# Kernel optimization log

Measured on AMD Instinct MI355X. Metric: run time of the kernel, lower is better.

The kernel has to match this reference:

```python
import jax, jax.numpy as jnp
import numpy as np

B, Wd, C, H, F = 48, 88, 256, 32, 1024
NH_SELF, NH_CROSS = 8, 8


def _ln(x, g, b, eps=1e-5):
    mu = x.mean(-1, keepdims=True)
    var = ((x - mu) ** 2).mean(-1, keepdims=True)
    return (x - mu) / jnp.sqrt(var + eps) * g + b


def setup_inputs() -> dict:
    key = jax.random.key(0)
    ks = jax.random.split(key, 16)
    s = 0.02  # weight init scale
    d = {
        'pooled_features': jax.random.normal(ks[0], (B, Wd, C), jnp.float32),
        'features': jax.random.normal(ks[1], (B, C, H, Wd), jnp.float32),
        'self_pe': jax.random.normal(ks[2], (Wd, C), jnp.float32),
        'cross_pe': jax.random.normal(ks[3], (H, C), jnp.float32),
    }
    # LayerNorm params
    for n in ['ln_qs', 'ln_vs', 'ln_qc', 'ln_kv', 'ln_vc', 'ln_ffn']:
        d[n + '_g'] = jnp.ones((C,), jnp.float32)
        d[n + '_b'] = jnp.zeros((C,), jnp.float32)
    # attention projections (stored [in,out]; y = x @ W + b)
    names = ['Wq_s', 'Wk_s', 'Wv_s', 'Wp_s', 'Wq_c', 'Wk_c', 'Wv_c', 'Wp_c']
    for i, n in enumerate(names):
        d[n] = jax.random.normal(ks[4 + i], (C, C), jnp.float32) * s
    for n in ['bq_s', 'bv_s', 'bp_s', 'bq_c', 'bv_c', 'bp_c']:
        d[n] = jnp.zeros((C,), jnp.float32)
    # FFN
    d['W1'] = jax.random.normal(ks[12], (C, F), jnp.float32) * s
    d['b1'] = jnp.zeros((F,), jnp.float32)
    d['W2'] = jax.random.normal(ks[13], (F, C), jnp.float32) * s
    d['b2'] = jnp.zeros((C,), jnp.float32)
    return d


def reference(pooled_features, features, self_pe, cross_pe,
              ln_qs_g, ln_qs_b, ln_vs_g, ln_vs_b,
              ln_qc_g, ln_qc_b, ln_kv_g, ln_kv_b, ln_vc_g, ln_vc_b,
              ln_ffn_g, ln_ffn_b,
              Wq_s, bq_s, Wk_s, Wv_s, bv_s, Wp_s, bp_s,
              Wq_c, bq_c, Wk_c, Wv_c, bv_c, Wp_c, bp_c,
              W1, b1, W2, b2):
    b, w, c = pooled_features.shape
    h = features.shape[2]
    ds = c // NH_SELF
    dc = c // NH_CROSS

    # ---- cross attention first (op_order='cross_first', with_pe=True) ----
    xq = pooled_features                                  # [B,W,C]
    qn = _ln(xq, ln_qc_g, ln_qc_b)
    kv = jnp.transpose(features, (0, 3, 2, 1))            # [B,W,H,C]
    kn = _ln(kv + cross_pe[None, None], ln_kv_g, ln_kv_b)
    vn = _ln(kv, ln_vc_g, ln_vc_b)
    q = (qn @ Wq_c + bq_c).reshape(b, w, NH_CROSS, dc)    # query len 1 per column
    k = (kn @ Wk_c).reshape(b, w, h, NH_CROSS, dc)
    v = (vn @ Wv_c + bv_c).reshape(b, w, h, NH_CROSS, dc)
    attn = jnp.einsum('bwhd,bwkhd->bwhk', q, k) * (dc ** -0.5)
    attn = jax.nn.softmax(attn, axis=-1)
    out = jnp.einsum('bwhk,bwkhd->bwhd', attn, v).reshape(b, w, c)
    x = out @ Wp_c + bp_c + xq

    # ---- self attention over width tokens ----
    qn = _ln(x + self_pe[None], ln_qs_g, ln_qs_b)
    vn = _ln(x, ln_vs_g, ln_vs_b)
    q = (qn @ Wq_s + bq_s).reshape(b, w, NH_SELF, ds)
    k = (qn @ Wk_s).reshape(b, w, NH_SELF, ds)
    v = (vn @ Wv_s + bv_s).reshape(b, w, NH_SELF, ds)
    attn = jnp.einsum('bnhd,bmhd->bhnm', q, k) * (ds ** -0.5)
    attn = jax.nn.softmax(attn, axis=-1)
    out = jnp.einsum('bhnm,bmhd->bnhd', attn, v).reshape(b, w, c)
    x = out @ Wp_s + bp_s + x

    # ---- FFN (mmcv FFN, num_fcs=2, GELU, identity residual) ----
    hdn = _ln(x, ln_ffn_g, ln_ffn_b)
    hdn = jax.nn.gelu(hdn @ W1 + b1, approximate=False) @ W2 + b2
    return x + hdn
```

## Files before the change

### kernel.cpp

```cpp
#include <hip/hip_runtime.h>
#include <math.h>

#define B_   48
#define W_   88
#define C_   256
#define H_   32
#define F_   1024
#define BW_  (B_ * W_)
#define BWH_ (B_ * W_ * H_)
#define HW_  (H_ * W_)

typedef float  f32x4  __attribute__((ext_vector_type(4)));
typedef __bf16 bf16x8 __attribute__((ext_vector_type(8)));

__device__ __forceinline__ unsigned short f2bf(float f) {
  union { float f; unsigned int u; } v; v.f = f;
  unsigned int r = v.u + 0x7FFFu + ((v.u >> 16) & 1u);
  return (unsigned short)(r >> 16);
}
__device__ __forceinline__ float bf2f(unsigned short h) {
  union { unsigned int u; float f; } v; v.u = ((unsigned int)h) << 16;
  return v.f;
}
__device__ __forceinline__ unsigned int pack2(float a, float b) {
  return (unsigned int)f2bf(a) | ((unsigned int)f2bf(b) << 16);
}

__global__ __launch_bounds__(256) void prep_all(
    const float* __restrict__ Wq_s, const float* __restrict__ Wk_s,
    const float* __restrict__ Wv_s, const float* __restrict__ Wp_s,
    const float* __restrict__ W1, const float* __restrict__ W2,
    const float* __restrict__ Wq_c, const float* __restrict__ Wk_c,
    const float* __restrict__ Wv_c, const float* __restrict__ Wp_c,
    const float* __restrict__ bq_s, const float* __restrict__ bv_s,
    const float* __restrict__ bq_c, const float* __restrict__ bv_c,
    const float* __restrict__ bp_c,
    const float* __restrict__ pooled,
    const float* __restrict__ ln_qc_g, const float* __restrict__ ln_qc_b,
    const float* __restrict__ cross_pe,
    unsigned short* __restrict__ wqkvs, unsigned short* __restrict__ wps,
    unsigned short* __restrict__ w1t, unsigned short* __restrict__ w2t,
    unsigned short* __restrict__ mqk, unsigned short* __restrict__ mvp,
    float* __restrict__ bqk, float* __restrict__ bvp,
    float* __restrict__ bqkvs, unsigned short* __restrict__ qn_c,
    float* __restrict__ pes) {
  __shared__ float smem[256 * 33 + 4 * 33];
  int blk = blockIdx.x, t = threadIdx.x;

  if (blk < 768) {
    const float* src; unsigned short* dst; int Cc, R, tile;
    if (blk < 64)       { src = Wq_s; dst = wqkvs;          Cc = 256;  R = 256;  tile = blk; }
    else if (blk < 128) { src = Wk_s; dst = wqkvs + 65536;  Cc = 256;  R = 256;  tile = blk - 64; }
    else if (blk < 192) { src = Wv_s; dst = wqkvs + 131072; Cc = 256;  R = 256;  tile = blk - 128; }
    else if (blk < 256) { src = Wp_s; dst = wps;            Cc = 256;  R = 256;  tile = blk - 192; }
    else if (blk < 512) { src = W1;   dst = w1t;            Cc = 1024; R = 256;  tile = blk - 256; }
    else                { src = W2;   dst = w2t;            Cc = 256;  R = 1024; tile = blk - 512; }
    int tcn = Cc >> 5;
    int tr = tile / tcn, tc = tile % tcn;
    float (*lds)[33] = (float(*)[33])smem;
    int r = t >> 3, c4 = (t & 7) * 4;
    float4 v = *(const float4*)(src + (size_t)(tr * 32 + r) * Cc + tc * 32 + c4);
    lds[r][c4 + 0] = v.x; lds[r][c4 + 1] = v.y; lds[r][c4 + 2] = v.z; lds[r][c4 + 3] = v.w;
    __syncthreads();
    int rd = t >> 3, cd4 = (t & 7) * 4;
    unsigned int u0 = pack2(lds[cd4 + 0][rd], lds[cd4 + 1][rd]);
    unsigned int u1 = pack2(lds[cd4 + 2][rd], lds[cd4 + 3][rd]);
    uint2 u; u.x = u0; u.y = u1;
    *(uint2*)(dst + (size_t)(tc * 32 + rd) * R + tr * 32 + cd4) = u;
  } else if (blk < 1280) {
    int lb = blk - 768;
    int h = lb >> 6, cb = lb & 63;
    float (*wq)[33] = (float(*)[33])smem;
    float (*wk)[33] = (float(*)[33])(smem + 256 * 33);
#pragma unroll
    for (int p = 0; p < 8; p++) {
      int dp = (t >> 3) + 32 * p, d4 = (t & 7) * 4;
      float4 v = *(const float4*)(Wq_c + (size_t)dp * 256 + 32 * h + d4);
      wq[dp][d4 + 0] = v.x; wq[dp][d4 + 1] = v.y; wq[dp][d4 + 2] = v.z; wq[dp][d4 + 3] = v.w;
    }
    if (t < 128) {
      int c_l = t >> 5, dd = t & 31;
      wk[c_l][dd] = Wk_c[(size_t)(cb * 4 + c_l) * 256 + 32 * h + dd];
    }
    __syncthreads();
    const float scale = 0.17677669529663689f;
    int c_l = t >> 6, ln = t & 63;
    int n = 256 * h + cb * 4 + c_l;
#pragma unroll
    for (int j = 0; j < 4; j++) {
      int dp = ln + 64 * j;
      float acc = 0.f;
#pragma unroll
      for (int dd = 0; dd < 32; dd++) acc += wq[dp][dd] * wk[c_l][dd];
      mqk[(size_t)n * 256 + dp] = f2bf(acc * scale);
    }
    if (ln == 0) {
      float bb = 0.f;
#pragma unroll
      for (int dd = 0; dd < 32; dd++) bb += bq_c[32 * h + dd] * wk[c_l][dd];
      bqk[n] = bb * scale;
    }
  } else if (blk < 1792) {
    int lb = blk - 1280;
    int h = lb >> 6, db = lb & 63;
    float (*wv)[33] = (float(*)[33])smem;
    float (*wp)[33] = (float(*)[33])(smem + 256 * 33);
#pragma unroll
    for (int p = 0; p < 8; p++) {
      int c = (t >> 3) + 32 * p, d4 = (t & 7) * 4;
      float4 v = *(const float4*)(Wv_c + (size_t)c * 256 + 32 * h + d4);
      wv[c][d4 + 0] = v.x; wv[c][d4 + 1] = v.y; wv[c][d4 + 2] = v.z; wv[c][d4 + 3] = v.w;
    }
    if (t < 128) {
      int d_l = t >> 5, dd = t & 31;
      wp[d_l][dd] = Wp_c[(size_t)(32 * h + dd) * 256 + db * 4 + d_l];
    }
    __syncthreads();
    int d_l = t >> 6, ln = t & 63;
    int d = db * 4 + d_l;
#pragma unroll
    for (int j = 0; j < 4; j++) {
      int c = ln + 64 * j;
      float acc = 0.f;
#pragma unroll
      for (int dd = 0; dd < 32; dd++) acc += wv[c][dd] * wp[d_l][dd];
      mvp[(size_t)d * 2048 + 256 * h + c] = f2bf(acc);
    }
  } else if (blk == 1792) {
    float acc = bp_c[t];
    for (int dp = 0; dp < 256; dp++) acc += bv_c[dp] * Wp_c[(size_t)dp * 256 + t];
    bvp[t] = acc;
    bqkvs[t] = bq_s[t]; bqkvs[256 + t] = 0.f; bqkvs[512 + t] = bv_s[t];
  } else if (blk < 6017) {
    int row = blk - 1793, c = t;
    float v = pooled[(size_t)row * C_ + c];
    float s1 = v, s2 = v * v;
#pragma unroll
    for (int m = 32; m > 0; m >>= 1) {
      s1 += __shfl_xor(s1, m, 64); s2 += __shfl_xor(s2, m, 64);
    }
    float* red = smem;
    int wave = c >> 6;
    if ((c & 63) == 0) { red[wave] = s1; red[4 + wave] = s2; }
    __syncthreads();
    s1 = red[0] + red[1] + red[2] + red[3];
    s2 = red[4] + red[5] + red[6] + red[7];
    float mu = s1 * (1.f / C_);
    float rs = rsqrtf(s2 * (1.f / C_) - mu * mu + 1e-5f);
    qn_c[(size_t)row * C_ + c] = f2bf((v - mu) * rs * ln_qc_g[c] + ln_qc_b[c]);
  } else {
    int h = t >> 3, seg = t & 7;
    const float* pr = cross_pe + (size_t)h * 256 + seg * 32;
    float s1 = 0.f, s2 = 0.f;
#pragma unroll
    for (int i = 0; i < 32; i++) { float v = pr[i]; s1 += v; s2 += v * v; }
    s1 += __shfl_xor(s1, 1, 8); s2 += __shfl_xor(s2, 1, 8);
    s1 += __shfl_xor(s1, 2, 8); s2 += __shfl_xor(s2, 2, 8);
    s1 += __shfl_xor(s1, 4, 8); s2 += __shfl_xor(s2, 4, 8);
    if (seg == 0) { pes[2 * h] = s1; pes[2 * h + 1] = s2; }
  }
}

__global__ __launch_bounds__(128, 2) void cross_fused(
    const float* __restrict__ features, const float* __restrict__ cross_pe,
    const unsigned short* __restrict__ qt_g,
    const float* __restrict__ g_kv, const float* __restrict__ b_kv,
    const float* __restrict__ g_vc, const float* __restrict__ b_vc,
    const float* __restrict__ pes,
    unsigned short* __restrict__ ctx_g) {
  __shared__ __attribute__((aligned(16))) float stage[2 * 4 * 268];
  const int p = blockIdx.x;
  const int xcd = p & 7, slot = p >> 3;
  const int b = xcd + 8 * (slot / 22);
  const int w0 = (slot % 22) * 4;
  const int t = threadIdx.x;
  const int bw0 = b * 88 + w0;
  const int w = t >> 5, c8 = t & 31, cbase = c8 << 3;

  float qg[8][8], Qg[8], Qb[8];
  {
    float gk8[8], bk8[8];
    float4 u0 = *(const float4*)(g_kv + cbase), u1 = *(const float4*)(g_kv + cbase + 4);
    gk8[0]=u0.x; gk8[1]=u0.y; gk8[2]=u0.z; gk8[3]=u0.w;
    gk8[4]=u1.x; gk8[5]=u1.y; gk8[6]=u1.z; gk8[7]=u1.w;
    u0 = *(const float4*)(b_kv + cbase); u1 = *(const float4*)(b_kv + cbase + 4);
    bk8[0]=u0.x; bk8[1]=u0.y; bk8[2]=u0.z; bk8[3]=u0.w;
    bk8[4]=u1.x; bk8[5]=u1.y; bk8[6]=u1.z; bk8[7]=u1.w;
    const unsigned short* qrow = qt_g + (size_t)(bw0 + w) * 2048 + cbase;
#pragma unroll
    for (int hd = 0; hd < 8; hd++) {
      bf16x8 qv = *(const bf16x8*)(qrow + hd * 256);
      float sg = 0.f, sb = 0.f;
#pragma unroll
      for (int i = 0; i < 8; i++) {
        float qf = (float)qv[i];
        qg[hd][i] = qf * gk8[i];
        sg += qg[hd][i];
        sb += qf * bk8[i];
      }
      Qg[hd] = sg; Qb[hd] = sb;
    }
#pragma unroll
    for (int m = 1; m < 32; m <<= 1) {
#pragma unroll
      for (int hd = 0; hd < 8; hd++) {
        Qg[hd] += __shfl_xor(Qg[hd], m, 32);
        Qb[hd] += __shfl_xor(Qb[hd], m, 32);
      }
    }
  }

  float accA[8][8];
  float accB[8], l[8];
#pragma unroll
  for (int hd = 0; hd < 8; hd++) {
    accB[hd] = 0.f; l[hd] = 0.f;
#pragma unroll
    for (int i = 0; i < 8; i++) accA[hd][i] = 0.f;
  }

  const float* fbase = features + (size_t)b * (C_ * HW_) + w0;
  float4 x0 = *(const float4*)(fbase + (size_t)t * HW_);
  float4 x1 = *(const float4*)(fbase + (size_t)(t + 128) * HW_);
  float4 y0 = *(const float4*)(fbase + (size_t)t * HW_ + 88);
  float4 y1 = *(const float4*)(fbase + (size_t)(t + 128) * HW_ + 88);

  float peC[8];
  {
    float4 q0 = *(const float4*)(cross_pe + cbase);
    float4 q1 = *(const float4*)(cross_pe + cbase + 4);
    peC[0]=q0.x; peC[1]=q0.y; peC[2]=q0.z; peC[3]=q0.w;
    peC[4]=q1.x; peC[5]=q1.y; peC[6]=q1.z; peC[7]=q1.w;
  }
  float pesC1 = pes[0], pesC2 = pes[1];

  float ps1, ps2, pu, pS[8], vprev[8];

  {
    float* st = stage;
    st[0 * 268 + t] = x0.x; st[1 * 268 + t] = x0.y;
    st[2 * 268 + t] = x0.z; st[3 * 268 + t] = x0.w;
    st[0 * 268 + 128 + t] = x1.x; st[1 * 268 + 128 + t] = x1.y;
    st[2 * 268 + 128 + t] = x1.z; st[3 * 268 + 128 + t] = x1.w;
    asm volatile("s_waitcnt lgkmcnt(0)" ::: "memory");
    __builtin_amdgcn_s_barrier();
    asm volatile("" ::: "memory");
    x0 = *(const float4*)(fbase + (size_t)t * HW_ + 2 * 88);
    x1 = *(const float4*)(fbase + (size_t)(t + 128) * HW_ + 2 * 88);
    const float* sr = st + w * 268 + cbase;
    float4 v0 = *(const float4*)(sr);
    float4 v1 = *(const float4*)(sr + 4);
    float vls[8] = {v0.x, v0.y, v0.z, v0.w, v1.x, v1.y, v1.z, v1.w};
    float peN[8];
    {
      float4 q0 = *(const float4*)(cross_pe + 256 + cbase);
      float4 q1 = *(const float4*)(cross_pe + 256 + cbase + 4);
      peN[0]=q0.x; peN[1]=q0.y; peN[2]=q0.z; peN[3]=q0.w;
      peN[4]=q1.x; peN[5]=q1.y; peN[6]=q1.z; peN[7]=q1.w;
    }
    float s1 = 0.f, s2 = 0.f, sp = 0.f, vp[8];
#pragma unroll
    for (int i = 0; i < 8; i++) {
      float v = vls[i];
      vp[i] = v + peC[i];
      s1 += v; s2 += v * v; sp += v * peC[i];
    }
#pragma unroll
    for (int hd = 0; hd < 8; hd++) {
      float a = 0.f;
#pragma unroll
      for (int i = 0; i < 8; i++) a += qg[hd][i] * vp[i];
      pS[hd] = a;
    }
    ps1 = s1; ps2 = s2; pu = s2 + 2.f * sp;
#pragma unroll
    for (int i = 0; i < 8; i++) vprev[i] = vls[i];
    float4 t0 = x0, t1 = x1;
    x0 = y0; x1 = y1; y0 = t0; y1 = t1;
#pragma unroll
    for (int i = 0; i < 8; i++) peC[i] = peN[i];
  }

  for (int h = 1; h < 32; ++h) {
    float* st = stage + (h & 1) * (4 * 268);
    st[0 * 268 + t] = x0.x; st[1 * 268 + t] = x0.y;
    st[2 * 268 + t] = x0.z; st[3 * 268 + t] = x0.w;
    st[0 * 268 + 128 + t] = x1.x; st[1 * 268 + 128 + t] = x1.y;
    st[2 * 268 + 128 + t] = x1.z; st[3 * 268 + 128 + t] = x1.w;
    asm volatile("s_waitcnt lgkmcnt(0)" ::: "memory");
    __builtin_amdgcn_s_barrier();
    asm volatile("" ::: "memory");
    if (h < 30) {
      x0 = *(const float4*)(fbase + (size_t)t * HW_ + (h + 2) * 88);
      x1 = *(const float4*)(fbase + (size_t)(t + 128) * HW_ + (h + 2) * 88);
    }
    const float* sr = st + w * 268 + cbase;
    float4 v0 = *(const float4*)(sr);
    float4 v1 = *(const float4*)(sr + 4);
#pragma unroll
    for (int m = 1; m < 32; m <<= 1) {
      ps1 += __shfl_xor(ps1, m, 32);
      ps2 += __shfl_xor(ps2, m, 32);
      pu  += __shfl_xor(pu, m, 32);
#pragma unroll
      for (int hd = 0; hd < 8; hd++) pS[hd] += __shfl_xor(pS[hd], m, 32);
    }
    float peN[8];
    if (h < 31) {
      float4 q0 = *(const float4*)(cross_pe + (h + 1) * 256 + cbase);
      float4 q1 = *(const float4*)(cross_pe + (h + 1) * 256 + cbase + 4);
      peN[0]=q0.x; peN[1]=q0.y; peN[2]=q0.z; peN[3]=q0.w;
      peN[4]=q1.x; peN[5]=q1.y; peN[6]=q1.z; peN[7]=q1.w;
    } else {
#pragma unroll
      for (int i = 0; i < 8; i++) peN[i] = 0.f;
    }
    float vls[8] = {v0.x, v0.y, v0.z, v0.w, v1.x, v1.y, v1.z, v1.w};
    float s1 = 0.f, s2 = 0.f, sp = 0.f, vp[8];
#pragma unroll
    for (int i = 0; i < 8; i++) {
      float v = vls[i];
      vp[i] = v + peC[i];
      s1 += v; s2 += v * v; sp += v * peC[i];
    }
    float nS[8];
#pragma unroll
    for (int hd = 0; hd < 8; hd++) {
      float a = 0.f;
#pragma unroll
      for (int i = 0; i < 8; i++) a += qg[hd][i] * vp[i];
      nS[hd] = a;
    }
    {
      float mu_v = ps1 * (1.f / 256.f);
      float rs_v = rsqrtf(ps2 * (1.f / 256.f) - mu_v * mu_v + 1e-5f);
      float mu_k = (ps1 + pesC1) * (1.f / 256.f);
      float rs_k = rsqrtf((pu + pesC2) * (1.f / 256.f) - mu_k * mu_k + 1e-5f);
#pragma unroll
      for (int hd = 0; hd < 8; hd++) {
        float sc = rs_k * (pS[hd] - mu_k * Qg[hd]) + Qb[hd];
        float e = __expf(sc);
        float er = e * rs_v;
        l[hd] += e;
        accB[hd] += er * mu_v;
#pragma unroll
        for (int i = 0; i < 8; i++) accA[hd][i] += er * vprev[i];
      }
    }
    ps1 = s1; ps2 = s2; pu = s2 + 2.f * sp;
#pragma unroll
    for (int hd = 0; hd < 8; hd++) pS[hd] = nS[hd];
#pragma unroll
    for (int i = 0; i < 8; i++) { vprev[i] = vls[i]; peC[i] = peN[i]; }
    pesC1 = pes[2 * h]; pesC2 = pes[2 * h + 1];
    float4 t0 = x0, t1 = x1;
    x0 = y0; x1 = y1; y0 = t0; y1 = t1;
  }

  {
#pragma unroll
    for (int m = 1; m < 32; m <<= 1) {
      ps1 += __shfl_xor(ps1, m, 32);
      ps2 += __shfl_xor(ps2, m, 32);
      pu  += __shfl_xor(pu, m, 32);
#pragma unroll
      for (int hd = 0; hd < 8; hd++) pS[hd] += __shfl_xor(pS[hd], m, 32);
    }
    float mu_v = ps1 * (1.f / 256.f);
    float rs_v = rsqrtf(ps2 * (1.f / 256.f) - mu_v * mu_v + 1e-5f);
    float mu_k = (ps1 + pesC1) * (1.f / 256.f);
    float rs_k = rsqrtf((pu + pesC2) * (1.f / 256.f) - mu_k * mu_k + 1e-5f);
#pragma unroll
    for (int hd = 0; hd < 8; hd++) {
      float sc = rs_k * (pS[hd] - mu_k * Qg[hd]) + Qb[hd];
      float e = __expf(sc);
      float er = e * rs_v;
      l[hd] += e;
      accB[hd] += er * mu_v;
#pragma unroll
      for (int i = 0; i < 8; i++) accA[hd][i] += er * vprev[i];
    }
  }

  float gv8[8], bv8[8];
  {
    float4 u0 = *(const float4*)(g_vc + cbase), u1 = *(const float4*)(g_vc + cbase + 4);
    gv8[0]=u0.x; gv8[1]=u0.y; gv8[2]=u0.z; gv8[3]=u0.w;
    gv8[4]=u1.x; gv8[5]=u1.y; gv8[6]=u1.z; gv8[7]=u1.w;
    u0 = *(const float4*)(b_vc + cbase); u1 = *(const float4*)(b_vc + cbase + 4);
    bv8[0]=u0.x; bv8[1]=u0.y; bv8[2]=u0.z; bv8[3]=u0.w;
    bv8[4]=u1.x; bv8[5]=u1.y; bv8[6]=u1.z; bv8[7]=u1.w;
  }
  unsigned short* orow = ctx_g + (size_t)(bw0 + w) * 2048 + cbase;
#pragma unroll
  for (int hd = 0; hd < 8; hd++) {
    float inv = 1.f / l[hd];
    unsigned short pk[8];
#pragma unroll
    for (int i = 0; i < 8; i++)
      pk[i] = f2bf(gv8[i] * (accA[hd][i] - accB[hd]) * inv + bv8[i]);
    *(uint4*)(orow + hd * 256) = *(uint4*)pk;
  }
}

__global__ __launch_bounds__(256) void ln_rows(
    const float* __restrict__ x,
    const float* __restrict__ g, const float* __restrict__ bta,
    unsigned short* __restrict__ out) {
  int row = blockIdx.x, c = threadIdx.x;
  float v = x[(size_t)row * C_ + c];
  float s1 = v, s2 = v * v;
#pragma unroll
  for (int m = 32; m > 0; m >>= 1) {
    s1 += __shfl_xor(s1, m, 64);
    s2 += __shfl_xor(s2, m, 64);
  }
  __shared__ float red[8];
  int wave = c >> 6;
  if ((c & 63) == 0) { red[wave] = s1; red[4 + wave] = s2; }
  __syncthreads();
  s1 = red[0] + red[1] + red[2] + red[3];
  s2 = red[4] + red[5] + red[6] + red[7];
  float mu = s1 * (1.f / C_);
  float rs = rsqrtf(s2 * (1.f / C_) - mu * mu + 1e-5f);
  out[(size_t)row * C_ + c] = f2bf((v - mu) * rs * g[c] + bta[c]);
}

__global__ __launch_bounds__(256) void ln_dual(
    const float* __restrict__ x, const float* __restrict__ pe,
    const float* __restrict__ g1, const float* __restrict__ b1a,
    const float* __restrict__ g2, const float* __restrict__ b2a,
    unsigned short* __restrict__ out1, unsigned short* __restrict__ out2) {
  int row = blockIdx.x, c = threadIdx.x;
  float v = x[(size_t)row * C_ + c];
  float vp = v + pe[(size_t)(row % 88) * C_ + c];
  float s1 = v, s2 = v * v, t1 = vp, t2 = vp * vp;
#pragma unroll
  for (int m = 32; m > 0; m >>= 1) {
    s1 += __shfl_xor(s1, m, 64); s2 += __shfl_xor(s2, m, 64);
    t1 += __shfl_xor(t1, m, 64); t2 += __shfl_xor(t2, m, 64);
  }
  __shared__ float red[16];
  int wave = c >> 6;
  if ((c & 63) == 0) {
    red[wave] = s1; red[4 + wave] = s2; red[8 + wave] = t1; red[12 + wave] = t2;
  }
  __syncthreads();
  s1 = red[0] + red[1] + red[2] + red[3];
  s2 = red[4] + red[5] + red[6] + red[7];
  t1 = red[8] + red[9] + red[10] + red[11];
  t2 = red[12] + red[13] + red[14] + red[15];
  float mu = s1 * (1.f / C_), rs = rsqrtf(s2 * (1.f / C_) - mu * mu + 1e-5f);
  float mup = t1 * (1.f / C_), rsp = rsqrtf(t2 * (1.f / C_) - mup * mup + 1e-5f);
  out1[(size_t)row * C_ + c] = f2bf((vp - mup) * rsp * g1[c] + b1a[c]);
  out2[(size_t)row * C_ + c] = f2bf((v - mu) * rs * g2[c] + b2a[c]);
}

__global__ __launch_bounds__(256) void gemm_bt(
    const unsigned short* __restrict__ A, const unsigned short* __restrict__ Bt,
    int M, int N, int K,
    const float* __restrict__ bias, const float* __restrict__ resid,
    float* __restrict__ outF, unsigned short* __restrict__ outB, int act_gelu) {
  __shared__ __attribute__((aligned(16))) unsigned short As[64][32];
  __shared__ __attribute__((aligned(16))) unsigned short Bs[64][32];
  const int tiles_n = N >> 6;
  const int bm = blockIdx.x / tiles_n;
  const int bn = blockIdx.x % tiles_n;
  const int tid = threadIdx.x;
  const int wave = tid >> 6, lane = tid & 63;
  const int quad = lane >> 4, lr = lane & 15;
  const int wm = (wave >> 1) << 5, wn = (wave & 1) << 5;
  const int lrow = tid >> 2;
  const int lcol = (tid & 3) << 3;
  const size_t a_base = (size_t)(bm * 64 + lrow) * K + lcol;
  const size_t b_base = (size_t)(bn * 64 + lrow) * K + lcol;
  f32x4 acc[2][2] = {};
  uint4 areg = *(const uint4*)(A + a_base);
  uint4 breg = *(const uint4*)(Bt + b_base);
  for (int k0 = 0; k0 < K; k0 += 32) {
    *(uint4*)&As[lrow][lcol] = areg;
    *(uint4*)&Bs[lrow][lcol] = breg;
    __syncthreads();
    if (k0 + 32 < K) {
      areg = *(const uint4*)(A + a_base + k0 + 32);
      breg = *(const uint4*)(Bt + b_base + k0 + 32);
    }
    bf16x8 af0 = *(const bf16x8*)&As[wm + lr][quad << 3];
    bf16x8 af1 = *(const bf16x8*)&As[wm + 16 + lr][quad << 3];
    bf16x8 bf0 = *(const bf16x8*)&Bs[wn + lr][quad << 3];
    bf16x8 bf1 = *(const bf16x8*)&Bs[wn + 16 + lr][quad << 3];
    acc[0][0] = __builtin_amdgcn_mfma_f32_16x16x32_bf16(af0, bf0, acc[0][0], 0, 0, 0);
    acc[0][1] = __builtin_amdgcn_mfma_f32_16x16x32_bf16(af0, bf1, acc[0][1], 0, 0, 0);
    acc[1][0] = __builtin_amdgcn_mfma_f32_16x16x32_bf16(af1, bf0, acc[1][0], 0, 0, 0);
    acc[1][1] = __builtin_amdgcn_mfma_f32_16x16x32_bf16(af1, bf1, acc[1][1], 0, 0, 0);
    __syncthreads();
  }
#pragma unroll
  for (int i = 0; i < 2; i++)
#pragma unroll
    for (int j = 0; j < 2; j++)
#pragma unroll
      for (int rr = 0; rr < 4; rr++) {
        int row = bm * 64 + wm + i * 16 + quad * 4 + rr;
        int col = bn * 64 + wn + j * 16 + lr;
        float val = acc[i][j][rr];
        if (bias) val += bias[col];
        if (act_gelu) val = 0.5f * val * (1.f + erff(val * 0.70710678118654752f));
        if (resid) val += resid[(size_t)row * N + col];
        if (outF) outF[(size_t)row * N + col] = val;
        else outB[(size_t)row * N + col] = f2bf(val);
      }
}

__global__ __launch_bounds__(256) void gemm_bt_st(
    const unsigned short* __restrict__ A, const unsigned short* __restrict__ Bt,
    int M, int N, int K, int ldc,
    const float* __restrict__ bias, float* __restrict__ outF) {
  __shared__ __attribute__((aligned(16))) unsigned short As[64][32];
  __shared__ __attribute__((aligned(16))) unsigned short Bs[64][32];
  const int tiles_n = N >> 6;
  const int bm = blockIdx.x / tiles_n;
  const int bn = blockIdx.x % tiles_n;
  const int tid = threadIdx.x;
  const int wave = tid >> 6, lane = tid & 63;
  const int quad = lane >> 4, lr = lane & 15;
  const int wm = (wave >> 1) << 5, wn = (wave & 1) << 5;
  const int lrow = tid >> 2;
  const int lcol = (tid & 3) << 3;
  const size_t a_base = (size_t)(bm * 64 + lrow) * K + lcol;
  const size_t b_base = (size_t)(bn * 64 + lrow) * K + lcol;
  f32x4 acc[2][2] = {};
  uint4 areg = *(const uint4*)(A + a_base);
  uint4 breg = *(const uint4*)(Bt + b_base);
  for (int k0 = 0; k0 < K; k0 += 32) {
    *(uint4*)&As[lrow][lcol] = areg;
    *(uint4*)&Bs[lrow][lcol] = breg;
    __syncthreads();
    if (k0 + 32 < K) {
      areg = *(const uint4*)(A + a_base + k0 + 32);
      breg = *(const uint4*)(Bt + b_base + k0 + 32);
    }
    bf16x8 af0 = *(const bf16x8*)&As[wm + lr][quad << 3];
    bf16x8 af1 = *(const bf16x8*)&As[wm + 16 + lr][quad << 3];
    bf16x8 bf0 = *(const bf16x8*)&Bs[wn + lr][quad << 3];
    bf16x8 bf1 = *(const bf16x8*)&Bs[wn + 16 + lr][quad << 3];
    acc[0][0] = __builtin_amdgcn_mfma_f32_16x16x32_bf16(af0, bf0, acc[0][0], 0, 0, 0);
    acc[0][1] = __builtin_amdgcn_mfma_f32_16x16x32_bf16(af0, bf1, acc[0][1], 0, 0, 0);
    acc[1][0] = __builtin_amdgcn_mfma_f32_16x16x32_bf16(af1, bf0, acc[1][0], 0, 0, 0);
    acc[1][1] = __builtin_amdgcn_mfma_f32_16x16x32_bf16(af1, bf1, acc[1][1], 0, 0, 0);
    __syncthreads();
  }
#pragma unroll
  for (int i = 0; i < 2; i++)
#pragma unroll
    for (int j = 0; j < 2; j++)
#pragma unroll
      for (int rr = 0; rr < 4; rr++) {
        int row = bm * 64 + wm + i * 16 + quad * 4 + rr;
        int col = bn * 64 + wn + j * 16 + lr;
        outF[(size_t)row * ldc + col] = acc[i][j][rr] + bias[col];
      }
}

__global__ __launch_bounds__(192) void self_attn3(
    const float* __restrict__ qkv, unsigned short* __restrict__ out) {
  int b = blockIdx.x >> 3;
  int h = blockIdx.x & 7;
  int t = threadIdx.x;
  __shared__ float kl[88][33];
  __shared__ float vl[88][33];
  for (int i = t; i < 704; i += 192) {
    int m = i >> 3, d4 = (i & 7) << 2;
    float4 kv4 = *(const float4*)(qkv + (size_t)(b * 88 + m) * 768 + 256 + h * 32 + d4);
    float4 vv4 = *(const float4*)(qkv + (size_t)(b * 88 + m) * 768 + 512 + h * 32 + d4);
    kl[m][d4 + 0] = kv4.x; kl[m][d4 + 1] = kv4.y; kl[m][d4 + 2] = kv4.z; kl[m][d4 + 3] = kv4.w;
    vl[m][d4 + 0] = vv4.x; vl[m][d4 + 1] = vv4.y; vl[m][d4 + 2] = vv4.z; vl[m][d4 + 3] = vv4.w;
  }
  __syncthreads();
  int r = t >> 1, dh = t & 1;
  if (r < 88) {
    const float* qrow = qkv + (size_t)(b * 88 + r) * 768 + h * 32;
    float qr[32];
#pragma unroll
    for (int g = 0; g < 8; g++) {
      float4 q4 = *(const float4*)(qrow + g * 4);
      qr[g * 4 + 0] = q4.x; qr[g * 4 + 1] = q4.y; qr[g * 4 + 2] = q4.z; qr[g * 4 + 3] = q4.w;
    }
    float sreg[44];
    float mx = -1e30f;
    int m0 = dh * 44;
    for (int mi = 0; mi < 44; mi++) {
      const float* krow = kl[m0 + mi];
      float s = 0.f;
#pragma unroll
      for (int d = 0; d < 32; d++) s += qr[d] * krow[d];
      s *= 0.17677669529663689f;
      sreg[mi] = s;
      mx = fmaxf(mx, s);
    }
    mx = fmaxf(mx, __shfl_xor(mx, 1, 64));
    float sum = 0.f;
    for (int mi = 0; mi < 44; mi++) { float e = __expf(sreg[mi] - mx); sreg[mi] = e; sum += e; }
    sum += __shfl_xor(sum, 1, 64);
    float inv = 1.f / sum;
    float o[32];
#pragma unroll
    for (int d = 0; d < 32; d++) o[d] = 0.f;
    for (int mi = 0; mi < 44; mi++) {
      float p = sreg[mi] * inv;
      const float* vrow = vl[m0 + mi];
#pragma unroll
      for (int d = 0; d < 32; d++) o[d] += p * vrow[d];
    }
#pragma unroll
    for (int d = 0; d < 32; d++) o[d] += __shfl_xor(o[d], 1, 64);
    unsigned short* orow = out + (size_t)(b * 88 + r) * 256 + h * 32 + dh * 16;
    uint4 u0, u1;
    int d0 = dh * 16;
    u0.x = pack2(o[d0 + 0], o[d0 + 1]);  u0.y = pack2(o[d0 + 2], o[d0 + 3]);
    u0.z = pack2(o[d0 + 4], o[d0 + 5]);  u0.w = pack2(o[d0 + 6], o[d0 + 7]);
    u1.x = pack2(o[d0 + 8], o[d0 + 9]);  u1.y = pack2(o[d0 + 10], o[d0 + 11]);
    u1.z = pack2(o[d0 + 12], o[d0 + 13]); u1.w = pack2(o[d0 + 14], o[d0 + 15]);
    *(uint4*)(orow) = u0;
    *(uint4*)(orow + 8) = u1;
  }
}

extern "C" void kernel_launch(void* const* d_in, const int* in_sizes, int n_in,
                              void* d_out, int out_size, void* d_ws, size_t ws_size,
                              hipStream_t stream) {
  (void)in_sizes; (void)n_in; (void)out_size; (void)ws_size;
  const float* pooled   = (const float*)d_in[0];
  const float* features = (const float*)d_in[1];
  const float* self_pe  = (const float*)d_in[2];
  const float* cross_pe = (const float*)d_in[3];
  const float* ln_qs_g = (const float*)d_in[4],  *ln_qs_b = (const float*)d_in[5];
  const float* ln_vs_g = (const float*)d_in[6],  *ln_vs_b = (const float*)d_in[7];
  const float* ln_qc_g = (const float*)d_in[8],  *ln_qc_b = (const float*)d_in[9];
  const float* ln_kv_g = (const float*)d_in[10], *ln_kv_b = (const float*)d_in[11];
  const float* ln_vc_g = (const float*)d_in[12], *ln_vc_b = (const float*)d_in[13];
  const float* ln_ffn_g = (const float*)d_in[14], *ln_ffn_b = (const float*)d_in[15];
  const float* Wq_s = (const float*)d_in[16], *Wk_s = (const float*)d_in[17];
  const float* Wv_s = (const float*)d_in[18], *Wp_s = (const float*)d_in[19];
  const float* Wq_c = (const float*)d_in[20], *Wk_c = (const float*)d_in[21];
  const float* Wv_c = (const float*)d_in[22], *Wp_c = (const float*)d_in[23];
  const float* bq_s = (const float*)d_in[24], *bv_s = (const float*)d_in[25];
  const float* bp_s = (const float*)d_in[26], *bq_c = (const float*)d_in[27];
  const float* bv_c = (const float*)d_in[28], *bp_c = (const float*)d_in[29];
  const float* W1 = (const float*)d_in[30], *b1 = (const float*)d_in[31];
  const float* W2 = (const float*)d_in[32], *b2 = (const float*)d_in[33];
  float* outp = (float*)d_out;
  char* ws = (char*)d_ws;

  size_t off = 0;
  auto alloc = [&](size_t bytes) { size_t o = off; off = (off + bytes + 255) & ~(size_t)255; return o; };
  size_t QT  = alloc((size_t)BW_ * 2048 * 2);
  size_t CTX = alloc((size_t)BW_ * 2048 * 2);
  size_t MQK = alloc((size_t)2048 * 256 * 2);
  size_t MVP = alloc((size_t)256 * 2048 * 2);
  size_t BQK = alloc(2048 * 4);
  size_t BVP = alloc(256 * 4);
  size_t WQKVS = alloc((size_t)768 * 256 * 2);
  size_t BQKVS = alloc(768 * 4);
  size_t WPS = alloc(65536 * 2);
  size_t W1T = alloc(262144 * 2), W2T = alloc(262144 * 2);
  size_t QN_C = alloc((size_t)BW_ * C_ * 2);
  size_t PES  = alloc(64 * 4);
  size_t X1    = alloc((size_t)BW_ * C_ * 4);
  size_t QN_S  = alloc((size_t)BW_ * C_ * 2);
  size_t VN_S  = alloc((size_t)BW_ * C_ * 2);
  size_t QKV_S = alloc((size_t)BW_ * 768 * 4);
  size_t S_O   = alloc((size_t)BW_ * C_ * 2);
  size_t X2    = alloc((size_t)BW_ * C_ * 4);
  size_t FFN   = alloc((size_t)BW_ * C_ * 2);
  size_t H1    = alloc((size_t)BW_ * F_ * 2);

  unsigned short* qt   = (unsigned short*)(ws + QT);
  unsigned short* ctx  = (unsigned short*)(ws + CTX);
  unsigned short* mqk  = (unsigned short*)(ws + MQK);
  unsigned short* mvp  = (unsigned short*)(ws + MVP);
  float* bqk = (float*)(ws + BQK);
  float* bvp = (float*)(ws + BVP);
  unsigned short* wqkvs = (unsigned short*)(ws + WQKVS);
  float* bqkvs = (float*)(ws + BQKVS);
  unsigned short* wps = (unsigned short*)(ws + WPS);
  unsigned short* w1t = (unsigned short*)(ws + W1T), *w2t = (unsigned short*)(ws + W2T);
  unsigned short* qn_c = (unsigned short*)(ws + QN_C);
  float* pes = (float*)(ws + PES);
  float*          x1   = (float*)(ws + X1);
  unsigned short* qn_s = (unsigned short*)(ws + QN_S);
  unsigned short* vn_s = (unsigned short*)(ws + VN_S);
  float* qkv_s = (float*)(ws + QKV_S);
  unsigned short* s_o  = (unsigned short*)(ws + S_O);
  float*          x2   = (float*)(ws + X2);
  unsigned short* ffn_n = (unsigned short*)(ws + FFN);
  unsigned short* h1    = (unsigned short*)(ws + H1);

  prep_all<<<6018, 256, 0, stream>>>(
      Wq_s, Wk_s, Wv_s, Wp_s, W1, W2, Wq_c, Wk_c, Wv_c, Wp_c,
      bq_s, bv_s, bq_c, bv_c, bp_c, pooled, ln_qc_g, ln_qc_b, cross_pe,
      wqkvs, wps, w1t, w2t, mqk, mvp, bqk, bvp, bqkvs, qn_c, pes);

  gemm_bt<<<(BW_ / 64) * (2048 / 64), 256, 0, stream>>>(qn_c, mqk, BW_, 2048, 256,
      bqk, nullptr, nullptr, qt, 0);

  cross_fused<<<1056, 128, 0, stream>>>(features, cross_pe, qt,
      ln_kv_g, ln_kv_b, ln_vc_g, ln_vc_b, pes, ctx);

  gemm_bt<<<(BW_ / 64) * (C_ / 64), 256, 0, stream>>>(ctx, mvp, BW_, C_, 2048,
      bvp, pooled, x1, nullptr, 0);

  ln_dual<<<BW_, 256, 0, stream>>>(x1, self_pe, ln_qs_g, ln_qs_b,
                                   ln_vs_g, ln_vs_b, qn_s, vn_s);

  gemm_bt_st<<<(BW_ / 64) * (512 / 64), 256, 0, stream>>>(qn_s, wqkvs, BW_, 512, 256,
      768, bqkvs, qkv_s);
  gemm_bt_st<<<(BW_ / 64) * (256 / 64), 256, 0, stream>>>(vn_s, wqkvs + 131072, BW_, 256, 256,
      768, bqkvs + 512, qkv_s + 512);

  self_attn3<<<B_ * 8, 192, 0, stream>>>(qkv_s, s_o);

  gemm_bt<<<(BW_ / 64) * (C_ / 64), 256, 0, stream>>>(s_o, wps, BW_, C_, C_,
      bp_s, x1, x2, nullptr, 0);

  ln_rows<<<BW_, 256, 0, stream>>>(x2, ln_ffn_g, ln_ffn_b, ffn_n);
  gemm_bt<<<(BW_ / 64) * (F_ / 64), 256, 0, stream>>>(ffn_n, w1t, BW_, F_, C_,
      b1, nullptr, nullptr, h1, 1);
  gemm_bt<<<(BW_ / 64) * (C_ / 64), 256, 0, stream>>>(h1, w2t, BW_, C_, F_,
      b2, x2, outp, nullptr, 0);
}
```

Before: 500.4 us.

## Split cross-attention over height halves with partial outputs and a merge kernel

The fused cross-attention kernel now processes only 16 of the 32 key rows per block, doubling the grid. Each block writes unnormalized fp32 partial context and softmax denominators to a workspace. A new merge kernel sums the two halves, normalizes, applies the value LayerNorm affine and writes bf16 context. The aim is more parallelism and a shorter serial loop per block, in exchange for extra fp32 workspace traffic and an additional launch.

```diff
diff --git a/kernel.cpp b/kernel.cpp
--- a/kernel.cpp
+++ b/kernel.cpp
@@ -9,6 +9,7 @@
 #define BW_  (B_ * W_)
 #define BWH_ (B_ * W_ * H_)
 #define HW_  (H_ * W_)
+#define NPSTR 2064
 
 typedef float  f32x4  __attribute__((ext_vector_type(4)));
 typedef __bf16 bf16x8 __attribute__((ext_vector_type(8)));
@@ -165,14 +166,16 @@
     const float* __restrict__ features, const float* __restrict__ cross_pe,
     const unsigned short* __restrict__ qt_g,
     const float* __restrict__ g_kv, const float* __restrict__ b_kv,
-    const float* __restrict__ g_vc, const float* __restrict__ b_vc,
     const float* __restrict__ pes,
-    unsigned short* __restrict__ ctx_g) {
+    float* __restrict__ np) {
   __shared__ __attribute__((aligned(16))) float stage[2 * 4 * 268];
   const int p = blockIdx.x;
   const int xcd = p & 7, slot = p >> 3;
-  const int b = xcd + 8 * (slot / 22);
-  const int w0 = (slot % 22) * 4;
+  const int b = xcd + 8 * (slot / 44);
+  const int rr = slot % 44;
+  const int half = rr / 22;
+  const int w0 = (rr % 22) * 4;
+  const int h0 = half << 4;
   const int t = threadIdx.x;
   const int bw0 = b * 88 + w0;
   const int w = t >> 5, c8 = t & 31, cbase = c8 << 3;
@@ -220,24 +223,24 @@
   }
 
   const float* fbase = features + (size_t)b * (C_ * HW_) + w0;
-  float4 x0 = *(const float4*)(fbase + (size_t)t * HW_);
-  float4 x1 = *(const float4*)(fbase + (size_t)(t + 128) * HW_);
-  float4 y0 = *(const float4*)(fbase + (size_t)t * HW_ + 88);
-  float4 y1 = *(const float4*)(fbase + (size_t)(t + 128) * HW_ + 88);
+  float4 x0 = *(const float4*)(fbase + (size_t)t * HW_ + h0 * 88);
+  float4 x1 = *(const float4*)(fbase + (size_t)(t + 128) * HW_ + h0 * 88);
+  float4 y0 = *(const float4*)(fbase + (size_t)t * HW_ + (h0 + 1) * 88);
+  float4 y1 = *(const float4*)(fbase + (size_t)(t + 128) * HW_ + (h0 + 1) * 88);
 
   float peC[8];
   {
-    float4 q0 = *(const float4*)(cross_pe + cbase);
-    float4 q1 = *(const float4*)(cross_pe + cbase + 4);
+    float4 q0 = *(const float4*)(cross_pe + h0 * 256 + cbase);
+    float4 q1 = *(const float4*)(cross_pe + h0 * 256 + cbase + 4);
     peC[0]=q0.x; peC[1]=q0.y; peC[2]=q0.z; peC[3]=q0.w;
     peC[4]=q1.x; peC[5]=q1.y; peC[6]=q1.z; peC[7]=q1.w;
   }
-  float pesC1 = pes[0], pesC2 = pes[1];
+  float pesC1 = pes[2 * h0], pesC2 = pes[2 * h0 + 1];
 
   float ps1, ps2, pu, pS[8], vprev[8];
 
   {
-    float* st = stage;
+    float* st = stage + (h0 & 1) * (4 * 268);
     st[0 * 268 + t] = x0.x; st[1 * 268 + t] = x0.y;
     st[2 * 268 + t] = x0.z; st[3 * 268 + t] = x0.w;
     st[0 * 268 + 128 + t] = x1.x; st[1 * 268 + 128 + t] = x1.y;
@@ -245,16 +248,16 @@
     asm volatile("s_waitcnt lgkmcnt(0)" ::: "memory");
     __builtin_amdgcn_s_barrier();
     asm volatile("" ::: "memory");
-    x0 = *(const float4*)(fbase + (size_t)t * HW_ + 2 * 88);
-    x1 = *(const float4*)(fbase + (size_t)(t + 128) * HW_ + 2 * 88);
+    x0 = *(const float4*)(fbase + (size_t)t * HW_ + (h0 + 2) * 88);
+    x1 = *(const float4*)(fbase + (size_t)(t + 128) * HW_ + (h0 + 2) * 88);
     const float* sr = st + w * 268 + cbase;
     float4 v0 = *(const float4*)(sr);
     float4 v1 = *(const float4*)(sr + 4);
     float vls[8] = {v0.x, v0.y, v0.z, v0.w, v1.x, v1.y, v1.z, v1.w};
     float peN[8];
     {
-      float4 q0 = *(const float4*)(cross_pe + 256 + cbase);
-      float4 q1 = *(const float4*)(cross_pe + 256 + cbase + 4);
+      float4 q0 = *(const float4*)(cross_pe + (h0 + 1) * 256 + cbase);
+      float4 q1 = *(const float4*)(cross_pe + (h0 + 1) * 256 + cbase + 4);
       peN[0]=q0.x; peN[1]=q0.y; peN[2]=q0.z; peN[3]=q0.w;
       peN[4]=q1.x; peN[5]=q1.y; peN[6]=q1.z; peN[7]=q1.w;
     }
@@ -281,7 +284,7 @@
     for (int i = 0; i < 8; i++) peC[i] = peN[i];
   }
 
-  for (int h = 1; h < 32; ++h) {
+  for (int h = h0 + 1; h < h0 + 16; ++h) {
     float* st = stage + (h & 1) * (4 * 268);
     st[0 * 268 + t] = x0.x; st[1 * 268 + t] = x0.y;
     st[2 * 268 + t] = x0.z; st[3 * 268 + t] = x0.w;
@@ -290,7 +293,7 @@
     asm volatile("s_waitcnt lgkmcnt(0)" ::: "memory");
     __builtin_amdgcn_s_barrier();
     asm volatile("" ::: "memory");
-    if (h < 30) {
+    if (h + 2 < h0 + 16) {
       x0 = *(const float4*)(fbase + (size_t)t * HW_ + (h + 2) * 88);
       x1 = *(const float4*)(fbase + (size_t)(t + 128) * HW_ + (h + 2) * 88);
     }
@@ -306,7 +309,7 @@
       for (int hd = 0; hd < 8; hd++) pS[hd] += __shfl_xor(pS[hd], m, 32);
     }
     float peN[8];
-    if (h < 31) {
+    if (h + 1 < h0 + 16) {
       float4 q0 = *(const float4*)(cross_pe + (h + 1) * 256 + cbase);
       float4 q1 = *(const float4*)(cross_pe + (h + 1) * 256 + cbase + 4);
       peN[0]=q0.x; peN[1]=q0.y; peN[2]=q0.z; peN[3]=q0.w;
@@ -382,25 +385,47 @@
     }
   }
 
-  float gv8[8], bv8[8];
-  {
-    float4 u0 = *(const float4*)(g_vc + cbase), u1 = *(const float4*)(g_vc + cbase + 4);
-    gv8[0]=u0.x; gv8[1]=u0.y; gv8[2]=u0.z; gv8[3]=u0.w;
-    gv8[4]=u1.x; gv8[5]=u1.y; gv8[6]=u1.z; gv8[7]=u1.w;
-    u0 = *(const float4*)(b_vc + cbase); u1 = *(const float4*)(b_vc + cbase + 4);
-    bv8[0]=u0.x; bv8[1]=u0.y; bv8[2]=u0.z; bv8[3]=u0.w;
-    bv8[4]=u1.x; bv8[5]=u1.y; bv8[6]=u1.z; bv8[7]=u1.w;
-  }
-  unsigned short* orow = ctx_g + (size_t)(bw0 + w) * 2048 + cbase;
+  float* nrow = np + ((size_t)(bw0 + w) * 2 + half) * NPSTR;
 #pragma unroll
   for (int hd = 0; hd < 8; hd++) {
-    float inv = 1.f / l[hd];
-    unsigned short pk[8];
-#pragma unroll
-    for (int i = 0; i < 8; i++)
-      pk[i] = f2bf(gv8[i] * (accA[hd][i] - accB[hd]) * inv + bv8[i]);
-    *(uint4*)(orow + hd * 256) = *(uint4*)pk;
-  }
+    float4 o0, o1;
+    o0.x = accA[hd][0] - accB[hd]; o0.y = accA[hd][1] - accB[hd];
+    o0.z = accA[hd][2] - accB[hd]; o0.w = accA[hd][3] - accB[hd];
+    o1.x = accA[hd][4] - accB[hd]; o1.y = accA[hd][5] - accB[hd];
+    o1.z = accA[hd][6] - accB[hd]; o1.w = accA[hd][7] - accB[hd];
+    *(float4*)(nrow + hd * 256 + cbase) = o0;
+    *(float4*)(nrow + hd * 256 + cbase + 4) = o1;
+  }
+  if (c8 == 0) {
+#pragma unroll
+    for (int hd = 0; hd < 8; hd++) nrow[2048 + hd] = l[hd];
+  }
+}
+
+__global__ __launch_bounds__(256) void merge_ctx(
+    const float* __restrict__ np, const float* __restrict__ g_vc,
+    const float* __restrict__ b_vc, unsigned short* __restrict__ ctx) {
+  int row = blockIdx.x, t = threadIdx.x;
+  int hd = t >> 5, c0 = (t & 31) << 3;
+  const float* n0 = np + (size_t)row * 2 * NPSTR;
+  const float* n1 = n0 + NPSTR;
+  float inv = 1.f / (n0[2048 + hd] + n1[2048 + hd]);
+  float4 a0 = *(const float4*)(n0 + hd * 256 + c0);
+  float4 a1 = *(const float4*)(n0 + hd * 256 + c0 + 4);
+  float4 b0 = *(const float4*)(n1 + hd * 256 + c0);
+  float4 b1 = *(const float4*)(n1 + hd * 256 + c0 + 4);
+  float4 g0 = *(const float4*)(g_vc + c0), g1 = *(const float4*)(g_vc + c0 + 4);
+  float4 v0 = *(const float4*)(b_vc + c0), v1 = *(const float4*)(b_vc + c0 + 4);
+  unsigned short pk[8];
+  pk[0] = f2bf(g0.x * (a0.x + b0.x) * inv + v0.x);
+  pk[1] = f2bf(g0.y * (a0.y + b0.y) * inv + v0.y);
+  pk[2] = f2bf(g0.z * (a0.z + b0.z) * inv + v0.z);
+  pk[3] = f2bf(g0.w * (a0.w + b0.w) * inv + v0.w);
+  pk[4] = f2bf(g1.x * (a1.x + b1.x) * inv + v1.x);
+  pk[5] = f2bf(g1.y * (a1.y + b1.y) * inv + v1.y);
+  pk[6] = f2bf(g1.z * (a1.z + b1.z) * inv + v1.z);
+  pk[7] = f2bf(g1.w * (a1.w + b1.w) * inv + v1.w);
+  *(uint4*)(ctx + (size_t)row * 2048 + hd * 256 + c0) = *(uint4*)pk;
 }
 
 __global__ __launch_bounds__(256) void ln_rows(
@@ -656,6 +681,7 @@
   auto alloc = [&](size_t bytes) { size_t o = off; off = (off + bytes + 255) & ~(size_t)255; return o; };
   size_t QT  = alloc((size_t)BW_ * 2048 * 2);
   size_t CTX = alloc((size_t)BW_ * 2048 * 2);
+  size_t NP  = alloc((size_t)BW_ * 2 * NPSTR * 4);
   size_t MQK = alloc((size_t)2048 * 256 * 2);
   size_t MVP = alloc((size_t)256 * 2048 * 2);
   size_t BQK = alloc(2048 * 4);
@@ -677,6 +703,7 @@
 
   unsigned short* qt   = (unsigned short*)(ws + QT);
   unsigned short* ctx  = (unsigned short*)(ws + CTX);
+  float*          np   = (float*)(ws + NP);
   unsigned short* mqk  = (unsigned short*)(ws + MQK);
   unsigned short* mvp  = (unsigned short*)(ws + MVP);
   float* bqk = (float*)(ws + BQK);
@@ -704,8 +731,10 @@
   gemm_bt<<<(BW_ / 64) * (2048 / 64), 256, 0, stream>>>(qn_c, mqk, BW_, 2048, 256,
       bqk, nullptr, nullptr, qt, 0);
 
-  cross_fused<<<1056, 128, 0, stream>>>(features, cross_pe, qt,
-      ln_kv_g, ln_kv_b, ln_vc_g, ln_vc_b, pes, ctx);
+  cross_fused<<<2112, 128, 0, stream>>>(features, cross_pe, qt,
+      ln_kv_g, ln_kv_b, pes, np);
+
+  merge_ctx<<<BW_, 256, 0, stream>>>(np, ln_vc_g, ln_vc_b, ctx);
 
   gemm_bt<<<(BW_ / 64) * (C_ / 64), 256, 0, stream>>>(ctx, mvp, BW_, C_, 2048,
       bvp, pooled, x1, nullptr, 0);
```

New measurement: 543.3 us. 1.09x slower.
